# Performance work log

Hardware: AMD Instinct MI355X
Metric: run time of the kernel (lower is better)

The kernel has to match this reference:

```python
import jax, jax.numpy as jnp
import numpy as np

B, S, E = 4, 2048, 1024
H = 16
D = E // H
WIN = 512


def setup_inputs() -> dict:
    key = jax.random.key(0)
    k1, k2, k3 = jax.random.split(key, 3)
    x = jax.random.normal(k1, (B, S, E), dtype=jnp.float32)
    w_in = jax.random.normal(k2, (3 * E, E), dtype=jnp.float32) * 0.02
    w_out = jax.random.normal(k3, (E, E), dtype=jnp.float32) * 0.02
    return {"x": x, "w_in": w_in, "w_out": w_out}


def _sliding_window_attention(q, k, v, win):
    b, h, s, d = q.shape
    nb = s // win
    scale = 1.0 / jnp.sqrt(jnp.float32(d))
    qb = q.reshape(b, h, nb, win, d)
    kb = k.reshape(b, h, nb, win, d)
    vb = v.reshape(b, h, nb, win, d)
    zpad = jnp.zeros_like(kb[:, :, :1])
    k2 = jnp.concatenate([jnp.concatenate([zpad, kb[:, :, :-1]], axis=2), kb], axis=3)  # [B,H,nb,2W,D]
    v2 = jnp.concatenate([jnp.concatenate([zpad, vb[:, :, :-1]], axis=2), vb], axis=3)
    scores = jnp.einsum('bhnqd,bhnkd->bhnqk', qb, k2) * scale  # [B,H,nb,W,2W]
    qi = jnp.arange(win)[:, None]          # query offset in block
    kj = jnp.arange(2 * win)[None, :]
    delta = qi - kj + win                  # q_idx - kv_idx
    valid = (delta >= 0) & (delta <= win)  # sliding-window causal mask
    blk = jnp.arange(nb)[:, None, None]
    valid = valid[None] & (blk * win + (kj[None] - win) >= 0)  # prev block invalid for block 0
    # ALiBi: bias = (q_idx - kv_idx) * exp2(-(h+1)*8/H)
    slopes = jnp.exp2(-(jnp.arange(H, dtype=jnp.float32) + 1.0) * 8.0 / H)  # [H]
    bias = slopes[:, None, None] * delta.astype(jnp.float32)  # [H,W,2W]
    scores = jnp.where(valid[None, :, :, :, :][:, None].squeeze(0)[None] if False else valid[None, None],
                       scores + bias[None, :, None], -jnp.inf)
    p = jax.nn.softmax(scores, axis=-1)
    out = jnp.einsum('bhnqk,bhnkd->bhnqd', p, v2)
    return out.reshape(b, h, s, d)


def reference(x, w_in, w_out):
    b, s, e = x.shape
    # packed in-projection (q is k is v path): split [3E,E] weight
    qkv = jnp.einsum('bse,fe->bsf', x, w_in)  # [B,S,3E]
    q, k, v = jnp.split(qkv, 3, axis=-1)
    def heads(t):
        return t.reshape(b, s, H, D).transpose(0, 2, 1, 3)  # [B,H,S,D]
    o = _sliding_window_attention(heads(q), heads(k), heads(v), WIN)  # [B,H,S,D]
    o = o.transpose(0, 2, 1, 3).reshape(b, s, e)
    return jnp.einsum('bse,fe->bsf', o, w_out)  # out_proj, batch-first output
```

## Files before the change

kernel.cpp:

```cpp
#include <hip/hip_runtime.h>
#include <hip/hip_bf16.h>


typedef __bf16 bf16x8 __attribute__((ext_vector_type(8)));
typedef float f32x4 __attribute__((ext_vector_type(4)));

__device__ __forceinline__ f32x4 mfma16(bf16x8 a, bf16x8 b, f32x4 c) {
    return __builtin_amdgcn_mfma_f32_16x16x32_bf16(a, b, c, 0, 0, 0);
}

__device__ __forceinline__ void gload_lds16(const void* g, void* l) {
    __builtin_amdgcn_global_load_lds(
        (const __attribute__((address_space(1))) unsigned int*)(unsigned long long)g,
        (__attribute__((address_space(3))) unsigned int*)(unsigned int)(unsigned long long)l,
        16, 0, 0);
}

__device__ __forceinline__ unsigned pkbf(float a, float b) {
    unsigned short ua = __builtin_bit_cast(unsigned short, (__bf16)a);
    unsigned short ub = __builtin_bit_cast(unsigned short, (__bf16)b);
    return (unsigned)ua | ((unsigned)ub << 16);
}

__global__ void init_flag(int* flag) { *flag = 0; }

__global__ void detect_f32(const unsigned short* __restrict__ w, int n, int* flag) {
    int i = blockIdx.x * blockDim.x + threadIdx.x;
    int hit = 0;
    for (; i < n; i += gridDim.x * blockDim.x) {
        int e = (w[i] >> 7) & 0xFF;
        if (e >= 0x8D) hit = 1;
    }
    unsigned long long m = __ballot(hit);
    if (m != 0 && (threadIdx.x & 63) == 0) atomicOr(flag, 1);
}

__global__ void cvt_all(const void* __restrict__ x, const void* __restrict__ wi,
                        const void* __restrict__ wo, __bf16* __restrict__ xb,
                        __bf16* __restrict__ wib, __bf16* __restrict__ wob,
                        const int* __restrict__ flag) {
    if (*flag == 0) return;
    const int XN = 8192 * 1024, WI = 3072 * 1024, WO = 1024 * 1024;
    const int stride = gridDim.x * blockDim.x;
    int i0 = blockIdx.x * blockDim.x + threadIdx.x;
    for (int j = i0; j < XN; j += stride) xb[j] = (__bf16)((const float*)x)[j];
    for (int j = i0; j < WI; j += stride) wib[j] = (__bf16)((const float*)wi)[j];
    for (int j = i0; j < WO; j += stride) wob[j] = (__bf16)((const float*)wo)[j];
}

__global__ __launch_bounds__(256, 3) void gemm_bt(
        const void* __restrict__ Araw, const __bf16* __restrict__ Acvt,
        const void* __restrict__ Braw, const __bf16* __restrict__ Bcvt,
        __bf16* __restrict__ Cb, float* __restrict__ Cf,
        const int* __restrict__ flagp, int M, int N, int K) {
    __shared__ __align__(16) __bf16 As[128 * 64];
    __shared__ __align__(16) __bf16 Bs[128 * 64];

    const int t = threadIdx.x;
    const int lane = t & 63;
    const int w = t >> 6;
    const int wr = w >> 1, wc = w & 1;
    const int q4 = lane >> 4, l16 = lane & 15;
    const int m0 = blockIdx.y * 128, n0 = blockIdx.x * 128;
    const bool isf32 = (*flagp != 0);
    const __bf16* A = isf32 ? Acvt : (const __bf16*)Araw;
    const __bf16* Bt = isf32 ? Bcvt : (const __bf16*)Braw;

    f32x4 acc[4][4] = {};

    const int lr = lane >> 3;
    const int lc = (lane & 7) ^ lr;

    for (int k0 = 0; k0 < K; k0 += 64) {
#pragma unroll
        for (int p = 0; p < 4; ++p) {
            int r0 = w * 32 + p * 8;
            gload_lds16(&A[(size_t)(m0 + r0 + lr) * K + k0 + lc * 8], &As[r0 * 64]);
            gload_lds16(&Bt[(size_t)(n0 + r0 + lr) * K + k0 + lc * 8], &Bs[r0 * 64]);
        }
        __syncthreads();

#pragma unroll
        for (int kt = 0; kt < 2; ++kt) {
            bf16x8 af[4], bfr[4];
#pragma unroll
            for (int mt = 0; mt < 4; ++mt) {
                int row = wr * 64 + mt * 16 + l16;
                af[mt] = *(const bf16x8*)&As[row * 64 + (((kt * 4 + q4) ^ (row & 7)) << 3)];
            }
#pragma unroll
            for (int nt = 0; nt < 4; ++nt) {
                int row = wc * 64 + nt * 16 + l16;
                bfr[nt] = *(const bf16x8*)&Bs[row * 64 + (((kt * 4 + q4) ^ (row & 7)) << 3)];
            }
#pragma unroll
            for (int mt = 0; mt < 4; ++mt)
#pragma unroll
                for (int nt = 0; nt < 4; ++nt)
                    acc[mt][nt] = mfma16(af[mt], bfr[nt], acc[mt][nt]);
        }
        __syncthreads();
    }

#pragma unroll
    for (int mt = 0; mt < 4; ++mt)
#pragma unroll
        for (int nt = 0; nt < 4; ++nt) {
            int col = n0 + wc * 64 + nt * 16 + l16;
#pragma unroll
            for (int r = 0; r < 4; ++r) {
                int row = m0 + wr * 64 + mt * 16 + q4 * 4 + r;
                if (Cf && isf32)
                    Cf[(size_t)row * N + col] = acc[mt][nt][r];
                else
                    Cb[(size_t)row * N + col] = (__bf16)acc[mt][nt][r];
            }
        }
}

__global__ __launch_bounds__(256, 2) void attn(
        const __bf16* __restrict__ qkv, __bf16* __restrict__ o) {
    __shared__ __align__(16) char smem[52224];
    __bf16* Ks  = (__bf16*)smem;
    __bf16* Vts = (__bf16*)(smem + 16384);
    __bf16* Ps  = (__bf16*)(smem + 33792);
    __bf16* Ot  = (__bf16*)smem;

    const int qt = blockIdx.x, h = blockIdx.y, b = blockIdx.z;
    const int t = threadIdx.x;
    const int lane = t & 63, w = t >> 6;
    const int q4 = lane >> 4, l16 = lane & 15;
    const int q0 = qt * 128, qw0 = q0 + w * 32;

    const float L2E = 1.4426950408889634f;
    const float slope2 = exp2f(-(float)(h + 1) * 0.5f) * L2E;
    const float scale2 = L2E * 0.125f;

    const int srow = t >> 3, scb = t & 7;
    const int ksoff = (scb ^ (srow & 7)) << 3;

    bf16x8 qf[2][2];
    const size_t qbase = ((size_t)b * 2048 + q0) * 3072 + (size_t)h * 64;
#pragma unroll
    for (int nt = 0; nt < 2; ++nt)
#pragma unroll
        for (int kt = 0; kt < 2; ++kt)
            qf[nt][kt] = *(const bf16x8*)&qkv[qbase +
                (size_t)(w * 32 + nt * 16 + l16) * 3072 + kt * 32 + q4 * 8];

    f32x4 O[4][2] = {};
    float mrow[2] = {-1e30f, -1e30f}, lrow[2] = {0.0f, 0.0f};

    const int nkt = (qt < 4 ? qt : 4) + 1;
    const int ktile0 = qt - (nkt - 1);
    const size_t bh = (size_t)b * 2048 * 3072 + (size_t)h * 64;

    uint4 kpre[4], vpre[4];

    {
        const size_t kb = bh + (size_t)(ktile0 * 128) * 3072 + 1024;
#pragma unroll
        for (int p = 0; p < 4; ++p)
            kpre[p] = *(const uint4*)&qkv[kb + (size_t)(p * 32 + srow) * 3072 + scb * 8];
#pragma unroll
        for (int p = 0; p < 4; ++p)
            vpre[p] = *(const uint4*)&qkv[kb + 1024 + (size_t)(p * 32 + srow) * 3072 + scb * 8];
#pragma unroll
        for (int p = 0; p < 4; ++p) {
            *(uint4*)&Ks[(p * 32 + srow) * 64 + ksoff] = kpre[p];
            const __bf16* ve = (const __bf16*)&vpre[p];
            int R = p * 4 + (srow >> 3);
#pragma unroll
            for (int j = 0; j < 8; ++j)
                Vts[(scb * 8 + j) * 136 + ((R ^ scb) << 3) + (srow & 7)] = ve[j];
        }
    }
    __syncthreads();

    for (int ki = 0; ki < nkt; ++ki) {
        const int k0 = (ktile0 + ki) * 128;
        if (ki + 1 < nkt) {
            const size_t kb = bh + (size_t)(k0 + 128) * 3072 + 1024;
#pragma unroll
            for (int p = 0; p < 4; ++p)
                kpre[p] = *(const uint4*)&qkv[kb + (size_t)(p * 32 + srow) * 3072 + scb * 8];
#pragma unroll
            for (int p = 0; p < 4; ++p)
                vpre[p] = *(const uint4*)&qkv[kb + 1024 + (size_t)(p * 32 + srow) * 3072 + scb * 8];
        }

#pragma unroll 1
        for (int hh = 0; hh < 2; ++hh) {
            const int ks0 = k0 + hh * 64;
            if (qw0 + 31 < ks0 || qw0 - 512 > ks0 + 63) continue;

            f32x4 sc[2][4] = {};
#pragma unroll
            for (int mt = 0; mt < 4; ++mt) {
                int krow = hh * 64 + mt * 16 + l16;
                bf16x8 ak0 = *(const bf16x8*)&Ks[krow * 64 + ((q4 ^ (l16 & 7)) << 3)];
                bf16x8 ak1 = *(const bf16x8*)&Ks[krow * 64 + (((4 + q4) ^ (l16 & 7)) << 3)];
                sc[0][mt] = mfma16(ak0, qf[0][0], sc[0][mt]);
                sc[0][mt] = mfma16(ak1, qf[0][1], sc[0][mt]);
                sc[1][mt] = mfma16(ak0, qf[1][0], sc[1][mt]);
                sc[1][mt] = mfma16(ak1, qf[1][1], sc[1][mt]);
            }

            float al[2];
#pragma unroll
            for (int nt = 0; nt < 2; ++nt) {
                const int qi = qw0 + nt * 16 + l16;
                const int db = qi - ks0 - q4 * 4;
                float tmx = -1e30f;
#pragma unroll
                for (int mt = 0; mt < 4; ++mt)
#pragma unroll
                    for (int r = 0; r < 4; ++r) {
                        int delta = db - mt * 16 - r;
                        float v = sc[nt][mt][r] * scale2 + slope2 * (float)delta;
                        v = ((unsigned)delta <= 512u) ? v : -1e30f;
                        sc[nt][mt][r] = v;
                        tmx = fmaxf(tmx, v);
                    }
                tmx = fmaxf(tmx, __shfl_xor(tmx, 16));
                tmx = fmaxf(tmx, __shfl_xor(tmx, 32));
                float mnew = fmaxf(mrow[nt], tmx);
                al[nt] = exp2f(mrow[nt] - mnew);
                mrow[nt] = mnew;
#pragma unroll
                for (int mtd = 0; mtd < 4; ++mtd)
                    O[mtd][nt] *= al[nt];
            }

            float rsum[2] = {0.0f, 0.0f};
#pragma unroll
            for (int nt = 0; nt < 2; ++nt) {
                int qrow = w * 32 + nt * 16 + l16;
#pragma unroll
                for (int mt = 0; mt < 4; ++mt) {
                    float p0 = exp2f(sc[nt][mt][0] - mrow[nt]);
                    float p1 = exp2f(sc[nt][mt][1] - mrow[nt]);
                    float p2 = exp2f(sc[nt][mt][2] - mrow[nt]);
                    float p3 = exp2f(sc[nt][mt][3] - mrow[nt]);
                    rsum[nt] += (p0 + p1) + (p2 + p3);
                    uint2 pk;
                    pk.x = pkbf(p0, p1);
                    pk.y = pkbf(p2, p3);
                    *(uint2*)&Ps[qrow * 72 + mt * 16 + q4 * 4] = pk;
                }
            }

#pragma unroll
            for (int kt = 0; kt < 2; ++kt) {
                bf16x8 bp0 = *(const bf16x8*)&Ps[(w * 32 + l16) * 72 + kt * 32 + q4 * 8];
                bf16x8 bp1 = *(const bf16x8*)&Ps[(w * 32 + 16 + l16) * 72 + kt * 32 + q4 * 8];
#pragma unroll
                for (int mtd = 0; mtd < 4; ++mtd) {
                    int d = mtd * 16 + l16;
                    int kb2 = (hh * 8 + kt * 4 + q4) ^ ((mtd * 2 + (l16 >> 3)) & 7);
                    bf16x8 av = *(const bf16x8*)&Vts[d * 136 + (kb2 << 3)];
                    O[mtd][0] = mfma16(av, bp0, O[mtd][0]);
                    O[mtd][1] = mfma16(av, bp1, O[mtd][1]);
                }
            }
#pragma unroll
            for (int nt = 0; nt < 2; ++nt) {
                float rs = rsum[nt];
                rs += __shfl_xor(rs, 16);
                rs += __shfl_xor(rs, 32);
                lrow[nt] = lrow[nt] * al[nt] + rs;
            }
        }

        __syncthreads();
        if (ki + 1 < nkt) {
#pragma unroll
            for (int p = 0; p < 4; ++p) {
                *(uint4*)&Ks[(p * 32 + srow) * 64 + ksoff] = kpre[p];
                const __bf16* ve = (const __bf16*)&vpre[p];
                int R = p * 4 + (srow >> 3);
#pragma unroll
                for (int j = 0; j < 8; ++j)
                    Vts[(scb * 8 + j) * 136 + ((R ^ scb) << 3) + (srow & 7)] = ve[j];
            }
        }
        __syncthreads();
    }

#pragma unroll
    for (int nt = 0; nt < 2; ++nt) {
        float inv = (lrow[nt] > 0.0f) ? 1.0f / lrow[nt] : 0.0f;
        int qrow = w * 32 + nt * 16 + l16;
#pragma unroll
        for (int mtd = 0; mtd < 4; ++mtd) {
            int chunk = (mtd * 2 + (q4 >> 1)) ^ (l16 & 7);
            uint2 pk;
            pk.x = pkbf(O[mtd][nt][0] * inv, O[mtd][nt][1] * inv);
            pk.y = pkbf(O[mtd][nt][2] * inv, O[mtd][nt][3] * inv);
            *(uint2*)&Ot[qrow * 64 + (chunk << 3) + (q4 & 1) * 4] = pk;
        }
    }
    const size_t obase = ((size_t)b * 2048 + q0) * 1024 + (size_t)h * 64;
#pragma unroll
    for (int i = 0; i < 4; ++i) {
        int u = i * 64 + lane;
        int row = u >> 3, ch = u & 7;
        int q = w * 32 + row;
        *(uint4*)&o[obase + (size_t)q * 1024 + ch * 8] =
            *(const uint4*)&Ot[q * 64 + ((ch ^ (row & 7)) << 3)];
    }
}

extern "C" void kernel_launch(void* const* d_in, const int* in_sizes, int n_in,
                              void* d_out, int out_size, void* d_ws, size_t ws_size,
                              hipStream_t stream) {
    char* ws = (char*)d_ws;
    int* flag = (int*)ws;
    size_t off = 256;
    __bf16* xb  = (__bf16*)(ws + off); off += (size_t)8192 * 1024 * 2;
    __bf16* wib = (__bf16*)(ws + off); off += (size_t)3072 * 1024 * 2;
    __bf16* wob = (__bf16*)(ws + off); off += (size_t)1024 * 1024 * 2;
    __bf16* qkv = (__bf16*)(ws + off); off += (size_t)8192 * 3072 * 2;
    __bf16* o   = (__bf16*)(ws + off);

    init_flag<<<1, 1, 0, stream>>>(flag);
    int nscan = in_sizes[2] < 65536 ? in_sizes[2] : 65536;
    detect_f32<<<16, 256, 0, stream>>>((const unsigned short*)d_in[2], nscan, flag);
    cvt_all<<<1024, 256, 0, stream>>>(d_in[0], d_in[1], d_in[2], xb, wib, wob, flag);

    gemm_bt<<<dim3(24, 64), 256, 0, stream>>>(d_in[0], xb, d_in[1], wib,
                                              qkv, nullptr, flag, 8192, 3072, 1024);
    attn<<<dim3(16, 16, 4), 256, 0, stream>>>(qkv, o);
    gemm_bt<<<dim3(8, 64), 256, 0, stream>>>(o, o, d_in[2], wob,
                                             (__bf16*)d_out, (float*)d_out, flag,
                                             8192, 1024, 1024);
}
```

Baseline: 266.4 us.

## Restructure attention: K from global, P in registers, double-buffered V, higher occupancy

The attention kernel no longer stages K in LDS; each wave reads K rows straight from global memory into MFMA operands. The P matrix stays in registers and feeds 16x16x16 MFMAs directly, so the Ps LDS round-trip goes away. V uses a double buffer in LDS, which lets one barrier per tile be dropped. LDS use shrinks so launch bounds allow 4 blocks per CU. It also skips masking on interior tiles, skips rescaling when the row max is unchanged, and adds s_setprio around MFMAs. The cost is more global/L2 traffic for K and the use of smaller-K MFMA instructions.

```diff
diff --git a/kernel.cpp b/kernel.cpp
--- a/kernel.cpp
+++ b/kernel.cpp
@@ -3,10 +3,24 @@
 
 
 typedef __bf16 bf16x8 __attribute__((ext_vector_type(8)));
+typedef __bf16 bf16x4 __attribute__((ext_vector_type(4)));
+typedef short short4v __attribute__((ext_vector_type(4)));
 typedef float f32x4 __attribute__((ext_vector_type(4)));
 
 __device__ __forceinline__ f32x4 mfma16(bf16x8 a, bf16x8 b, f32x4 c) {
     return __builtin_amdgcn_mfma_f32_16x16x32_bf16(a, b, c, 0, 0, 0);
+}
+
+__device__ __forceinline__ f32x4 mfma16k16(bf16x4 a, bf16x4 b, f32x4 c) {
+#if __has_builtin(__builtin_amdgcn_mfma_f32_16x16x16bf16_1k)
+    return __builtin_amdgcn_mfma_f32_16x16x16bf16_1k(
+        __builtin_bit_cast(short4v, a), __builtin_bit_cast(short4v, b), c, 0, 0, 0);
+#elif __has_builtin(__builtin_amdgcn_mfma_f32_16x16x16_bf16)
+    return __builtin_amdgcn_mfma_f32_16x16x16_bf16(a, b, c, 0, 0, 0);
+#else
+    asm("v_mfma_f32_16x16x16_bf16 %0, %1, %2, %0" : "+v"(c) : "v"(a), "v"(b));
+    return c;
+#endif
 }
 
 __device__ __forceinline__ void gload_lds16(const void* g, void* l) {
@@ -118,12 +132,10 @@
         }
 }
 
-__global__ __launch_bounds__(256, 2) void attn(
+__global__ __launch_bounds__(256, 4) void attn(
         const __bf16* __restrict__ qkv, __bf16* __restrict__ o) {
-    __shared__ __align__(16) char smem[52224];
-    __bf16* Ks  = (__bf16*)smem;
-    __bf16* Vts = (__bf16*)(smem + 16384);
-    __bf16* Ps  = (__bf16*)(smem + 33792);
+    __shared__ __align__(16) char smem[2 * 17408];
+    __bf16* Vts = (__bf16*)smem;
     __bf16* Ot  = (__bf16*)smem;
 
     const int qt = blockIdx.x, h = blockIdx.y, b = blockIdx.z;
@@ -137,7 +149,6 @@
     const float scale2 = L2E * 0.125f;
 
     const int srow = t >> 3, scb = t & 7;
-    const int ksoff = (scb ^ (srow & 7)) << 3;
 
     bf16x8 qf[2][2];
     const size_t qbase = ((size_t)b * 2048 + q0) * 3072 + (size_t)h * 64;
@@ -154,20 +165,17 @@
     const int nkt = (qt < 4 ? qt : 4) + 1;
     const int ktile0 = qt - (nkt - 1);
     const size_t bh = (size_t)b * 2048 * 3072 + (size_t)h * 64;
-
-    uint4 kpre[4], vpre[4];
+    const __bf16* Kg = qkv + bh + 1024 + (size_t)(q4 * 8);
+
+    uint4 vpre[4];
 
     {
-        const size_t kb = bh + (size_t)(ktile0 * 128) * 3072 + 1024;
+        const size_t vb = bh + (size_t)(ktile0 * 128) * 3072 + 2048;
 #pragma unroll
         for (int p = 0; p < 4; ++p)
-            kpre[p] = *(const uint4*)&qkv[kb + (size_t)(p * 32 + srow) * 3072 + scb * 8];
-#pragma unroll
-        for (int p = 0; p < 4; ++p)
-            vpre[p] = *(const uint4*)&qkv[kb + 1024 + (size_t)(p * 32 + srow) * 3072 + scb * 8];
+            vpre[p] = *(const uint4*)&qkv[vb + (size_t)(p * 32 + srow) * 3072 + scb * 8];
 #pragma unroll
         for (int p = 0; p < 4; ++p) {
-            *(uint4*)&Ks[(p * 32 + srow) * 64 + ksoff] = kpre[p];
             const __bf16* ve = (const __bf16*)&vpre[p];
             int R = p * 4 + (srow >> 3);
 #pragma unroll
@@ -179,109 +187,122 @@
 
     for (int ki = 0; ki < nkt; ++ki) {
         const int k0 = (ktile0 + ki) * 128;
+        const __bf16* Vb = Vts + (ki & 1) * 8704;
         if (ki + 1 < nkt) {
-            const size_t kb = bh + (size_t)(k0 + 128) * 3072 + 1024;
+            const size_t vb = bh + (size_t)(k0 + 128) * 3072 + 2048;
 #pragma unroll
             for (int p = 0; p < 4; ++p)
-                kpre[p] = *(const uint4*)&qkv[kb + (size_t)(p * 32 + srow) * 3072 + scb * 8];
-#pragma unroll
-            for (int p = 0; p < 4; ++p)
-                vpre[p] = *(const uint4*)&qkv[kb + 1024 + (size_t)(p * 32 + srow) * 3072 + scb * 8];
+                vpre[p] = *(const uint4*)&qkv[vb + (size_t)(p * 32 + srow) * 3072 + scb * 8];
         }
 
 #pragma unroll 1
         for (int hh = 0; hh < 2; ++hh) {
             const int ks0 = k0 + hh * 64;
             if (qw0 + 31 < ks0 || qw0 - 512 > ks0 + 63) continue;
-
-            f32x4 sc[2][4] = {};
-#pragma unroll
-            for (int mt = 0; mt < 4; ++mt) {
-                int krow = hh * 64 + mt * 16 + l16;
-                bf16x8 ak0 = *(const bf16x8*)&Ks[krow * 64 + ((q4 ^ (l16 & 7)) << 3)];
-                bf16x8 ak1 = *(const bf16x8*)&Ks[krow * 64 + (((4 + q4) ^ (l16 & 7)) << 3)];
-                sc[0][mt] = mfma16(ak0, qf[0][0], sc[0][mt]);
-                sc[0][mt] = mfma16(ak1, qf[0][1], sc[0][mt]);
-                sc[1][mt] = mfma16(ak0, qf[1][0], sc[1][mt]);
-                sc[1][mt] = mfma16(ak1, qf[1][1], sc[1][mt]);
-            }
-
-            float al[2];
+            const bool interior = (qw0 - ks0 >= 63) && (qw0 - ks0 <= 481);
+
+            uint2 pb[2][4];
+
 #pragma unroll
             for (int nt = 0; nt < 2; ++nt) {
+                f32x4 sc[4] = {};
+#pragma unroll
+                for (int mt = 0; mt < 4; ++mt) {
+                    const __bf16* kp = Kg + (size_t)(ks0 + mt * 16 + l16) * 3072;
+                    bf16x8 ak0 = *(const bf16x8*)kp;
+                    bf16x8 ak1 = *(const bf16x8*)(kp + 32);
+                    __builtin_amdgcn_s_setprio(1);
+                    sc[mt] = mfma16(ak0, qf[nt][0], sc[mt]);
+                    sc[mt] = mfma16(ak1, qf[nt][1], sc[mt]);
+                    __builtin_amdgcn_s_setprio(0);
+                }
+
                 const int qi = qw0 + nt * 16 + l16;
                 const int db = qi - ks0 - q4 * 4;
                 float tmx = -1e30f;
-#pragma unroll
-                for (int mt = 0; mt < 4; ++mt)
-#pragma unroll
-                    for (int r = 0; r < 4; ++r) {
-                        int delta = db - mt * 16 - r;
-                        float v = sc[nt][mt][r] * scale2 + slope2 * (float)delta;
-                        v = ((unsigned)delta <= 512u) ? v : -1e30f;
-                        sc[nt][mt][r] = v;
-                        tmx = fmaxf(tmx, v);
+                if (interior) {
+                    const float fb = slope2 * (float)db;
+#pragma unroll
+                    for (int mt = 0; mt < 4; ++mt) {
+                        float bm = fb - (float)(16 * mt) * slope2;
+#pragma unroll
+                        for (int r = 0; r < 4; ++r) {
+                            float v = fmaf(sc[mt][r], scale2, bm - (float)r * slope2);
+                            sc[mt][r] = v;
+                            tmx = fmaxf(tmx, v);
+                        }
                     }
+                } else {
+#pragma unroll
+                    for (int mt = 0; mt < 4; ++mt)
+#pragma unroll
+                        for (int r = 0; r < 4; ++r) {
+                            int delta = db - mt * 16 - r;
+                            float v = sc[mt][r] * scale2 + slope2 * (float)delta;
+                            v = ((unsigned)delta <= 512u) ? v : -1e30f;
+                            sc[mt][r] = v;
+                            tmx = fmaxf(tmx, v);
+                        }
+                }
                 tmx = fmaxf(tmx, __shfl_xor(tmx, 16));
                 tmx = fmaxf(tmx, __shfl_xor(tmx, 32));
-                float mnew = fmaxf(mrow[nt], tmx);
-                al[nt] = exp2f(mrow[nt] - mnew);
-                mrow[nt] = mnew;
-#pragma unroll
-                for (int mtd = 0; mtd < 4; ++mtd)
-                    O[mtd][nt] *= al[nt];
-            }
-
-            float rsum[2] = {0.0f, 0.0f};
-#pragma unroll
-            for (int nt = 0; nt < 2; ++nt) {
-                int qrow = w * 32 + nt * 16 + l16;
+
+                if (__any(tmx > mrow[nt])) {
+                    float mnew = fmaxf(mrow[nt], tmx);
+                    float al = exp2f(mrow[nt] - mnew);
+                    mrow[nt] = mnew;
+                    lrow[nt] *= al;
+#pragma unroll
+                    for (int mtd = 0; mtd < 4; ++mtd)
+                        O[mtd][nt] *= al;
+                }
+
+                float rs = 0.0f;
 #pragma unroll
                 for (int mt = 0; mt < 4; ++mt) {
-                    float p0 = exp2f(sc[nt][mt][0] - mrow[nt]);
-                    float p1 = exp2f(sc[nt][mt][1] - mrow[nt]);
-                    float p2 = exp2f(sc[nt][mt][2] - mrow[nt]);
-                    float p3 = exp2f(sc[nt][mt][3] - mrow[nt]);
-                    rsum[nt] += (p0 + p1) + (p2 + p3);
+                    float p0 = exp2f(sc[mt][0] - mrow[nt]);
+                    float p1 = exp2f(sc[mt][1] - mrow[nt]);
+                    float p2 = exp2f(sc[mt][2] - mrow[nt]);
+                    float p3 = exp2f(sc[mt][3] - mrow[nt]);
+                    rs += (p0 + p1) + (p2 + p3);
                     uint2 pk;
                     pk.x = pkbf(p0, p1);
                     pk.y = pkbf(p2, p3);
-                    *(uint2*)&Ps[qrow * 72 + mt * 16 + q4 * 4] = pk;
-                }
-            }
-
-#pragma unroll
-            for (int kt = 0; kt < 2; ++kt) {
-                bf16x8 bp0 = *(const bf16x8*)&Ps[(w * 32 + l16) * 72 + kt * 32 + q4 * 8];
-                bf16x8 bp1 = *(const bf16x8*)&Ps[(w * 32 + 16 + l16) * 72 + kt * 32 + q4 * 8];
-#pragma unroll
-                for (int mtd = 0; mtd < 4; ++mtd) {
-                    int d = mtd * 16 + l16;
-                    int kb2 = (hh * 8 + kt * 4 + q4) ^ ((mtd * 2 + (l16 >> 3)) & 7);
-                    bf16x8 av = *(const bf16x8*)&Vts[d * 136 + (kb2 << 3)];
-                    O[mtd][0] = mfma16(av, bp0, O[mtd][0]);
-                    O[mtd][1] = mfma16(av, bp1, O[mtd][1]);
-                }
-            }
-#pragma unroll
-            for (int nt = 0; nt < 2; ++nt) {
-                float rs = rsum[nt];
+                    pb[nt][mt] = pk;
+                }
                 rs += __shfl_xor(rs, 16);
                 rs += __shfl_xor(rs, 32);
-                lrow[nt] = lrow[nt] * al[nt] + rs;
-            }
-        }
-
-        __syncthreads();
+                lrow[nt] += rs;
+            }
+
+            const int dsw = l16 >> 3;
+#pragma unroll
+            for (int mtB = 0; mtB < 4; ++mtB) {
+                bf16x4 b0 = __builtin_bit_cast(bf16x4, pb[0][mtB]);
+                bf16x4 b1 = __builtin_bit_cast(bf16x4, pb[1][mtB]);
+                const int kc0 = hh * 8 + mtB * 2 + (q4 >> 1);
+#pragma unroll
+                for (int mtd = 0; mtd < 4; ++mtd) {
+                    int kc = kc0 ^ ((mtd * 2 + dsw) & 7);
+                    bf16x4 av = *(const bf16x4*)&Vb[(mtd * 16 + l16) * 136 +
+                                                    (kc << 3) + (q4 & 1) * 4];
+                    __builtin_amdgcn_s_setprio(1);
+                    O[mtd][0] = mfma16k16(av, b0, O[mtd][0]);
+                    O[mtd][1] = mfma16k16(av, b1, O[mtd][1]);
+                    __builtin_amdgcn_s_setprio(0);
+                }
+            }
+        }
+
         if (ki + 1 < nkt) {
+            __bf16* Vn = Vts + ((ki + 1) & 1) * 8704;
 #pragma unroll
             for (int p = 0; p < 4; ++p) {
-                *(uint4*)&Ks[(p * 32 + srow) * 64 + ksoff] = kpre[p];
                 const __bf16* ve = (const __bf16*)&vpre[p];
                 int R = p * 4 + (srow >> 3);
 #pragma unroll
                 for (int j = 0; j < 8; ++j)
-                    Vts[(scb * 8 + j) * 136 + ((R ^ scb) << 3) + (srow & 7)] = ve[j];
+                    Vn[(scb * 8 + j) * 136 + ((R ^ scb) << 3) + (srow & 7)] = ve[j];
             }
         }
         __syncthreads();
```

Result: slower. 364.7 us (+36.9%).
